# Kernel tuning notes

Hardware: AMD Instinct MI355X
Metric: run time of the kernel (lower is better)

## Reference

```python
import jax, jax.numpy as jnp
import numpy as np

H = 32        # num_attention_heads
KVH = 8       # num_key_value_heads
D = 2048      # hidden_size
HD = D // H   # head_dim = 64
GROUPS = H // KVH


def setup_inputs() -> dict:
    key = jax.random.key(0)
    k1, k2, k3, k4 = jax.random.split(key, 4)
    B, T = 2, 2048
    x = jax.random.normal(k1, (B, T, D), dtype=jnp.float32)
    wq = jax.random.normal(k2, (D, H * HD), dtype=jnp.float32) * (D ** -0.5)
    wkv = jax.random.normal(k3, (D, 2 * KVH * HD), dtype=jnp.float32) * (D ** -0.5)
    wo = jax.random.normal(k4, (H * HD, D), dtype=jnp.float32) * (D ** -0.5)
    return {"x": x, "wq": wq, "wkv": wkv, "wo": wo}


def reference(x, wq, wkv, wo):
    B, T, _ = x.shape
    scale = HD ** -0.5
    # projections
    q = (x @ wq).reshape(B, T, H, HD).transpose(0, 2, 1, 3)        # [B,H,T,hd]
    kv = x @ wkv                                                    # [B,T,2*KVH*hd]
    k, v = jnp.split(kv, 2, axis=-1)
    k = k.reshape(B, T, KVH, HD).transpose(0, 2, 1, 3)              # [B,KVH,T,hd]
    v = v.reshape(B, T, KVH, HD).transpose(0, 2, 1, 3)
    # repeat_interleave KV heads to match Q heads
    k = jnp.repeat(k, GROUPS, axis=1)                               # [B,H,T,hd]
    v = jnp.repeat(v, GROUPS, axis=1)
    scores = jnp.einsum('bhqd,bhkd->bhqk', q, k) * scale            # [B,H,T,T]
    causal = jnp.triu(jnp.ones((T, T), dtype=bool), k=1)
    scores = jnp.where(causal, -jnp.inf, scores)
    attn = jax.nn.softmax(scores, axis=-1)
    out = jnp.einsum('bhqk,bhkd->bhqd', attn, v)                    # [B,H,T,hd]
    out = out.transpose(0, 2, 1, 3).reshape(B, T, H * HD)
    return out @ wo
```

## Files before the change

### kernel.cpp

```cpp
#include <hip/hip_runtime.h>

using bf16   = __bf16;
using bf16x8 = __attribute__((ext_vector_type(8))) __bf16;
using f32x4  = __attribute__((ext_vector_type(4))) float;
using u32x4  = __attribute__((ext_vector_type(4))) unsigned;

#define T_SEQ 2048
#define NQKV 3072

__device__ __forceinline__ void async_cp16(const bf16* g, bf16* l) {
  __builtin_amdgcn_global_load_lds((__attribute__((address_space(1))) void*)(void*)g,
                                   (__attribute__((address_space(3))) void*)l, 16, 0, 0);
}

__global__ __launch_bounds__(256) void cvt_kernel(const float* __restrict__ in,
                                                  bf16* __restrict__ out) {
  long i = ((long)blockIdx.x * 256 + threadIdx.x) * 8;
  float4 a = *(const float4*)(in + i);
  float4 c = *(const float4*)(in + i + 4);
  bf16x8 v;
  v[0] = (bf16)a.x; v[1] = (bf16)a.y; v[2] = (bf16)a.z; v[3] = (bf16)a.w;
  v[4] = (bf16)c.x; v[5] = (bf16)c.y; v[6] = (bf16)c.z; v[7] = (bf16)c.w;
  *(bf16x8*)(out + i) = v;
}

__global__ __launch_bounds__(256) void transpose_cvt(const float* __restrict__ in,
                                                     bf16* __restrict__ out,
                                                     int R, int C) {
  __shared__ float tile[32][33];
  const int tc = blockIdx.x * 32;
  const int tr = blockIdx.y * 32;
  const int t = threadIdx.x;
  const int lr = t >> 5;
  const int lc = t & 31;
#pragma unroll
  for (int i = 0; i < 4; ++i)
    tile[lr + i * 8][lc] = in[(size_t)(tr + lr + i * 8) * C + tc + lc];
  __syncthreads();
#pragma unroll
  for (int i = 0; i < 4; ++i)
    out[(size_t)(tc + lr + i * 8) * R + tr + lc] = (bf16)tile[lc][lr + i * 8];
}

__global__ __launch_bounds__(256) void transpose_v(const bf16* __restrict__ in,
                                                   bf16* __restrict__ out) {
  __shared__ bf16 tile[32][33];
  const int c0 = blockIdx.x * 32;
  const int r0 = blockIdx.y * 32;
  const int t = threadIdx.x;
  const int lr = t >> 5;
  const int lc = t & 31;
#pragma unroll
  for (int i = 0; i < 4; ++i)
    tile[lr + i * 8][lc] = in[(size_t)(r0 + lr + i * 8) * NQKV + 2560 + c0 + lc];
  __syncthreads();
#pragma unroll
  for (int i = 0; i < 4; ++i) {
    int c = c0 + lr + i * 8;
    int r = r0 + lc;
    out[(size_t)((r >> 11) * 512 + c) * 2048 + (r & 2047)] = tile[lc][lr + i * 8];
  }
}

template <bool OUT_BF16>
__global__ __launch_bounds__(256, 3)
void gemm_kernel(const bf16* __restrict__ A, const bf16* __restrict__ Bt,
                 void* __restrict__ Cout, int Kdim, int Ndim) {
  __shared__ __attribute__((aligned(16))) bf16 As[128 * 64];
  __shared__ __attribute__((aligned(16))) bf16 Bs[128 * 64];
  const int tid  = threadIdx.x;
  const int lane = tid & 63;
  const int wave = tid >> 6;
  const int l16  = lane & 15;
  const int q4   = lane >> 4;
  const long m0 = (long)blockIdx.y * 128;
  const long n0 = (long)blockIdx.x * 128;
  const int wm = (wave >> 1) * 64;
  const int wn = (wave & 1) * 64;

  f32x4 acc[4][4] = {};

  for (int k0 = 0; k0 < Kdim; k0 += 64) {
    __syncthreads();
#pragma unroll
    for (int rr = 0; rr < 4; ++rr) {
      int ci  = rr * 256 + tid;
      int row = ci >> 3;
      int chp = ci & 7;
      int ch  = chp ^ (row & 7);
      async_cp16(A + (m0 + row) * (long)Kdim + k0 + ch * 8, &As[ci * 8]);
      async_cp16(Bt + (n0 + row) * (long)Kdim + k0 + ch * 8, &Bs[ci * 8]);
    }
    __syncthreads();
#pragma unroll
    for (int ks = 0; ks < 2; ++ks) {
      bf16x8 af[4], bfr[4];
#pragma unroll
      for (int mt = 0; mt < 4; ++mt) {
        int row = wm + mt * 16 + l16;
        int chp = (ks * 4 + q4) ^ (row & 7);
        af[mt] = *(const bf16x8*)&As[row * 64 + chp * 8];
      }
#pragma unroll
      for (int nt = 0; nt < 4; ++nt) {
        int row = wn + nt * 16 + l16;
        int chp = (ks * 4 + q4) ^ (row & 7);
        bfr[nt] = *(const bf16x8*)&Bs[row * 64 + chp * 8];
      }
#pragma unroll
      for (int mt = 0; mt < 4; ++mt)
#pragma unroll
        for (int nt = 0; nt < 4; ++nt)
          acc[mt][nt] = __builtin_amdgcn_mfma_f32_16x16x32_bf16(af[mt], bfr[nt],
                                                                acc[mt][nt], 0, 0, 0);
    }
  }
#pragma unroll
  for (int mt = 0; mt < 4; ++mt)
#pragma unroll
    for (int nt = 0; nt < 4; ++nt)
#pragma unroll
      for (int r = 0; r < 4; ++r) {
        long row = m0 + wm + mt * 16 + q4 * 4 + r;
        long col = n0 + wn + nt * 16 + l16;
        float v = acc[mt][nt][r];
        if constexpr (OUT_BF16)
          ((bf16*)Cout)[row * Ndim + col] = (bf16)v;
        else
          ((float*)Cout)[row * Ndim + col] = v;
      }
}

__global__ __launch_bounds__(256, 3)
void attn_kernel(const bf16* __restrict__ qkv, const bf16* __restrict__ vT,
                 bf16* __restrict__ outb) {
  __shared__ __attribute__((aligned(16))) bf16 Ks[64 * 64];
  __shared__ __attribute__((aligned(16))) bf16 Vs[64 * 64];

  const int tid  = threadIdx.x;
  const int lane = tid & 63;
  const int wave = tid >> 6;
  const int l16  = lane & 15;
  const int q4   = lane >> 4;

  const int bid = blockIdx.x;
  const int qt  = 15 - (bid >> 6);
  const int bh  = bid & 63;
  const int b   = bh >> 5;
  const int h   = bh & 31;
  const int kvh = h >> 2;
  const long rowbase = (long)b * T_SEQ;

  const int qrow0 = qt * 128;
  const int wq0   = qrow0 + wave * 32;
  const float cexp = 0.125f * 1.4426950408889634f;

  bf16x8 aq[2][2];
#pragma unroll
  for (int mt = 0; mt < 2; ++mt)
#pragma unroll
    for (int ks = 0; ks < 2; ++ks) {
      bf16x8 v = *(const bf16x8*)(qkv +
          (rowbase + wq0 + mt * 16 + l16) * (long)NQKV + h * 64 + ks * 32 + q4 * 8);
#pragma unroll
      for (int i = 0; i < 8; ++i) v[i] = (bf16)((float)v[i] * cexp);
      aq[mt][ks] = v;
    }

  bf16x8 ones_f;
#pragma unroll
  for (int i = 0; i < 8; ++i) ones_f[i] = (l16 == 0) ? (bf16)1.0f : (bf16)0.0f;

  f32x4 o[2][4] = {};
  f32x4 o_l[2] = {};

  const bf16* kbase = qkv + rowbase * (long)NQKV + 2048 + kvh * 64;
  const bf16* vbase = vT + ((long)b * 512 + kvh * 64) * 2048;

  for (int j0 = 0; j0 < qrow0 + 128; j0 += 64) {
    __syncthreads();
    {
#pragma unroll
      for (int h2 = 0; h2 < 2; ++h2) {
        int ci  = h2 * 256 + tid;
        int row = ci >> 3;
        int ch  = (ci & 7) ^ (row & 7);
        *(bf16x8*)&Ks[ci * 8] =
            *(const bf16x8*)(kbase + (long)(j0 + row) * NQKV + ch * 8);
        *(bf16x8*)&Vs[ci * 8] =
            *(const bf16x8*)(vbase + (long)row * 2048 + j0 + ch * 8);
      }
    }
    __syncthreads();
    if (j0 > wq0 + 31) continue;

    f32x4 s[2][4] = {};
#pragma unroll
    for (int ks = 0; ks < 2; ++ks) {
      bf16x8 bk[4];
#pragma unroll
      for (int nt = 0; nt < 4; ++nt) {
        int row  = nt * 16 + l16;
        int slot = (ks * 4 + q4) ^ (row & 7);
        bk[nt] = *(const bf16x8*)&Ks[row * 64 + slot * 8];
      }
#pragma unroll
      for (int mt = 0; mt < 2; ++mt)
#pragma unroll
        for (int nt = 0; nt < 4; ++nt)
          s[mt][nt] = __builtin_amdgcn_mfma_f32_16x16x32_bf16(bk[nt], aq[mt][ks],
                                                              s[mt][nt], 0, 0, 0);
    }

    if (j0 + 63 > wq0) {
#pragma unroll
      for (int mt = 0; mt < 2; ++mt)
#pragma unroll
        for (int nt = 0; nt < 4; ++nt)
#pragma unroll
          for (int r = 0; r < 4; ++r) {
            int rg = wq0 + mt * 16 + l16;
            int cg = j0 + nt * 16 + q4 * 4 + r;
            if (cg > rg) s[mt][nt][r] = -__builtin_inff();
          }
    }

    bf16x8 ap[2][2];
#pragma unroll
    for (int mt = 0; mt < 2; ++mt) {
      unsigned pk0, pk1, pk2, pk3, pk4, pk5, pk6, pk7;
      {
        float p0 = __builtin_amdgcn_exp2f(s[mt][0][0]);
        float p1 = __builtin_amdgcn_exp2f(s[mt][0][1]);
        float p2 = __builtin_amdgcn_exp2f(s[mt][0][2]);
        float p3 = __builtin_amdgcn_exp2f(s[mt][0][3]);
        asm("v_cvt_pk_bf16_f32 %0, %1, %2" : "=v"(pk0) : "v"(p0), "v"(p1));
        asm("v_cvt_pk_bf16_f32 %0, %1, %2" : "=v"(pk1) : "v"(p2), "v"(p3));
      }
      {
        float p0 = __builtin_amdgcn_exp2f(s[mt][1][0]);
        float p1 = __builtin_amdgcn_exp2f(s[mt][1][1]);
        float p2 = __builtin_amdgcn_exp2f(s[mt][1][2]);
        float p3 = __builtin_amdgcn_exp2f(s[mt][1][3]);
        asm("v_cvt_pk_bf16_f32 %0, %1, %2" : "=v"(pk2) : "v"(p0), "v"(p1));
        asm("v_cvt_pk_bf16_f32 %0, %1, %2" : "=v"(pk3) : "v"(p2), "v"(p3));
      }
      {
        float p0 = __builtin_amdgcn_exp2f(s[mt][2][0]);
        float p1 = __builtin_amdgcn_exp2f(s[mt][2][1]);
        float p2 = __builtin_amdgcn_exp2f(s[mt][2][2]);
        float p3 = __builtin_amdgcn_exp2f(s[mt][2][3]);
        asm("v_cvt_pk_bf16_f32 %0, %1, %2" : "=v"(pk4) : "v"(p0), "v"(p1));
        asm("v_cvt_pk_bf16_f32 %0, %1, %2" : "=v"(pk5) : "v"(p2), "v"(p3));
      }
      {
        float p0 = __builtin_amdgcn_exp2f(s[mt][3][0]);
        float p1 = __builtin_amdgcn_exp2f(s[mt][3][1]);
        float p2 = __builtin_amdgcn_exp2f(s[mt][3][2]);
        float p3 = __builtin_amdgcn_exp2f(s[mt][3][3]);
        asm("v_cvt_pk_bf16_f32 %0, %1, %2" : "=v"(pk6) : "v"(p0), "v"(p1));
        asm("v_cvt_pk_bf16_f32 %0, %1, %2" : "=v"(pk7) : "v"(p2), "v"(p3));
      }
      {
        unsigned a0 = pk0, b0 = pk2;
        asm("v_permlane32_swap_b32 %0, %1" : "+v"(a0), "+v"(b0));
        asm("v_permlane16_swap_b32 %0, %1" : "+v"(a0), "+v"(b0));
        unsigned a1 = pk1, b1 = pk3;
        asm("v_permlane32_swap_b32 %0, %1" : "+v"(a1), "+v"(b1));
        asm("v_permlane16_swap_b32 %0, %1" : "+v"(a1), "+v"(b1));
        u32x4 w; w.x = a0; w.y = a1; w.z = b0; w.w = b1;
        ap[mt][0] = __builtin_bit_cast(bf16x8, w);
      }
      {
        unsigned a0 = pk4, b0 = pk6;
        asm("v_permlane32_swap_b32 %0, %1" : "+v"(a0), "+v"(b0));
        asm("v_permlane16_swap_b32 %0, %1" : "+v"(a0), "+v"(b0));
        unsigned a1 = pk5, b1 = pk7;
        asm("v_permlane32_swap_b32 %0, %1" : "+v"(a1), "+v"(b1));
        asm("v_permlane16_swap_b32 %0, %1" : "+v"(a1), "+v"(b1));
        u32x4 w; w.x = a0; w.y = a1; w.z = b0; w.w = b1;
        ap[mt][1] = __builtin_bit_cast(bf16x8, w);
      }
    }

#pragma unroll
    for (int ks = 0; ks < 2; ++ks) {
      bf16x8 bv[4];
#pragma unroll
      for (int dt = 0; dt < 4; ++dt) {
        int row  = dt * 16 + l16;
        int slot = (ks * 4 + q4) ^ (row & 7);
        bv[dt] = *(const bf16x8*)&Vs[row * 64 + slot * 8];
      }
#pragma unroll
      for (int mt = 0; mt < 2; ++mt) {
#pragma unroll
        for (int dt = 0; dt < 4; ++dt)
          o[mt][dt] = __builtin_amdgcn_mfma_f32_16x16x32_bf16(ap[mt][ks], bv[dt],
                                                              o[mt][dt], 0, 0, 0);
        o_l[mt] = __builtin_amdgcn_mfma_f32_16x16x32_bf16(ap[mt][ks], ones_f,
                                                          o_l[mt], 0, 0, 0);
      }
    }
  }

#pragma unroll
  for (int mt = 0; mt < 2; ++mt) {
    float inv[4];
#pragma unroll
    for (int r = 0; r < 4; ++r) {
      float lsum = __shfl(o_l[mt][r], lane & 48);
      inv[r] = 1.0f / lsum;
    }
#pragma unroll
    for (int dt = 0; dt < 4; ++dt)
#pragma unroll
      for (int r = 0; r < 4; ++r) {
        long row = rowbase + wq0 + mt * 16 + q4 * 4 + r;
        int col = h * 64 + dt * 16 + l16;
        outb[row * 2048 + col] = (bf16)(o[mt][dt][r] * inv[r]);
      }
  }
}

extern "C" void kernel_launch(void* const* d_in, const int* in_sizes, int n_in,
                              void* d_out, int out_size, void* d_ws, size_t ws_size,
                              hipStream_t stream) {
  const float* x   = (const float*)d_in[0];
  const float* wq  = (const float*)d_in[1];
  const float* wkv = (const float*)d_in[2];
  const float* wo  = (const float*)d_in[3];
  float* out = (float*)d_out;
  char* ws = (char*)d_ws;

  bf16* xbf  = (bf16*)(ws + 0);
  bf16* w1   = (bf16*)(ws + 16777216);
  bf16* qkv  = (bf16*)(ws + 29360128);
  bf16* attn = xbf;
  bf16* vT   = w1;

  const size_t need_parallel = 54525952u + 8388608u;
  bf16* woT;
  bool woT_early;
  if (ws_size >= need_parallel) {
    woT = (bf16*)(ws + 54525952);
    woT_early = true;
  } else {
    woT = qkv;
    woT_early = false;
  }

  cvt_kernel<<<4096, 256, 0, stream>>>(x, xbf);
  transpose_cvt<<<dim3(64, 64), 256, 0, stream>>>(wq, w1, 2048, 2048);
  transpose_cvt<<<dim3(32, 64), 256, 0, stream>>>(wkv, w1 + 2048L * 2048, 2048, 1024);
  if (woT_early)
    transpose_cvt<<<dim3(64, 64), 256, 0, stream>>>(wo, woT, 2048, 2048);

  gemm_kernel<true><<<dim3(24, 32), 256, 0, stream>>>(xbf, w1, (void*)qkv, 2048, 3072);

  transpose_v<<<dim3(16, 128), 256, 0, stream>>>(qkv, vT);

  attn_kernel<<<1024, 256, 0, stream>>>(qkv, vT, attn);

  if (!woT_early)
    transpose_cvt<<<dim3(64, 64), 256, 0, stream>>>(wo, woT, 2048, 2048);

  gemm_kernel<false><<<dim3(16, 32), 256, 0, stream>>>(attn, woT, (void*)out, 2048, 2048);
}
```

Baseline: 258.9 us.

## Replace GEMM with 8-wave double-buffered larger-tile kernel with async prefetch

Replaces the 128x128 single-buffered GEMM with a 512-thread kernel using 256xBN tiles and double-buffered LDS. The next K tile loads asynchronously while MFMAs run on the current one, synchronised with explicit vmcnt waits and raw barriers, and MFMA phases get raised wave priority. This targets the exposed global-load latency and the redundant operand traffic of the smaller tiles, at the cost of more LDS and registers per block. It also means fewer blocks per GEMM (192 and 256), which could leave CUs underused.

```diff
diff --git a/kernel.cpp b/kernel.cpp
--- a/kernel.cpp
+++ b/kernel.cpp
@@ -62,63 +62,142 @@
   }
 }
 
-template <bool OUT_BF16>
-__global__ __launch_bounds__(256, 3)
-void gemm_kernel(const bf16* __restrict__ A, const bf16* __restrict__ Bt,
-                 void* __restrict__ Cout, int Kdim, int Ndim) {
-  __shared__ __attribute__((aligned(16))) bf16 As[128 * 64];
-  __shared__ __attribute__((aligned(16))) bf16 Bs[128 * 64];
+template <int KDIM, int BN, bool OUT_BF16>
+__global__ __launch_bounds__(512, 2)
+void gemm8_kernel(const bf16* __restrict__ A, const bf16* __restrict__ Bt,
+                  void* __restrict__ Cout, int Ndim) {
+  constexpr int NTILES = KDIM / 64;
+  constexpr int NFR = BN / 64;
+  __shared__ __attribute__((aligned(16))) bf16 As[2][256 * 64];
+  __shared__ __attribute__((aligned(16))) bf16 Bs[2][BN * 64];
+
   const int tid  = threadIdx.x;
   const int lane = tid & 63;
   const int wave = tid >> 6;
   const int l16  = lane & 15;
   const int q4   = lane >> 4;
-  const long m0 = (long)blockIdx.y * 128;
-  const long n0 = (long)blockIdx.x * 128;
-  const int wm = (wave >> 1) * 64;
-  const int wn = (wave & 1) * 64;
-
-  f32x4 acc[4][4] = {};
-
-  for (int k0 = 0; k0 < Kdim; k0 += 64) {
-    __syncthreads();
+  const int wm   = (wave >> 2) * 128;
+  const int wn   = (wave & 3) * (BN / 4);
+
+  const long m0 = (long)blockIdx.y * 256;
+  const long n0 = (long)blockIdx.x * BN;
+  const bf16* Ag = A + m0 * (long)KDIM;
+  const bf16* Bg = Bt + n0 * (long)KDIM;
+
+  f32x4 acc[8][NFR] = {};
+
+  auto stage = [&](int buf, int kt) {
+    const long k0 = (long)kt * 64;
 #pragma unroll
     for (int rr = 0; rr < 4; ++rr) {
-      int ci  = rr * 256 + tid;
+      int ci = rr * 512 + tid;
       int row = ci >> 3;
-      int chp = ci & 7;
-      int ch  = chp ^ (row & 7);
-      async_cp16(A + (m0 + row) * (long)Kdim + k0 + ch * 8, &As[ci * 8]);
-      async_cp16(Bt + (n0 + row) * (long)Kdim + k0 + ch * 8, &Bs[ci * 8]);
-    }
-    __syncthreads();
-#pragma unroll
-    for (int ks = 0; ks < 2; ++ks) {
-      bf16x8 af[4], bfr[4];
-#pragma unroll
-      for (int mt = 0; mt < 4; ++mt) {
-        int row = wm + mt * 16 + l16;
-        int chp = (ks * 4 + q4) ^ (row & 7);
-        af[mt] = *(const bf16x8*)&As[row * 64 + chp * 8];
-      }
-#pragma unroll
-      for (int nt = 0; nt < 4; ++nt) {
-        int row = wn + nt * 16 + l16;
-        int chp = (ks * 4 + q4) ^ (row & 7);
-        bfr[nt] = *(const bf16x8*)&Bs[row * 64 + chp * 8];
-      }
-#pragma unroll
-      for (int mt = 0; mt < 4; ++mt)
-#pragma unroll
-        for (int nt = 0; nt < 4; ++nt)
-          acc[mt][nt] = __builtin_amdgcn_mfma_f32_16x16x32_bf16(af[mt], bfr[nt],
-                                                                acc[mt][nt], 0, 0, 0);
-    }
+      int ch = (ci & 7) ^ (row & 7);
+      async_cp16(Ag + (long)row * KDIM + k0 + ch * 8, &As[buf][ci * 8]);
+    }
+#pragma unroll
+    for (int rr = 0; rr < BN / 64; ++rr) {
+      int ci = rr * 512 + tid;
+      int row = ci >> 3;
+      int ch = (ci & 7) ^ (row & 7);
+      async_cp16(Bg + (long)row * KDIM + k0 + ch * 8, &Bs[buf][ci * 8]);
+    }
+  };
+
+  stage(0, 0);
+  stage(1, 1);
+
+  for (int t = 0; t < NTILES; ++t) {
+    const int cur = t & 1;
+    if (t < NTILES - 1) {
+      if constexpr (BN == 256) asm volatile("s_waitcnt vmcnt(8)" ::: "memory");
+      else                     asm volatile("s_waitcnt vmcnt(6)" ::: "memory");
+    } else {
+      asm volatile("s_waitcnt vmcnt(0)" ::: "memory");
+    }
+    __builtin_amdgcn_s_barrier();
+
+    bf16x8 a0[4], b0[NFR];
+#pragma unroll
+    for (int mt = 0; mt < 4; ++mt) {
+      int row = wm + mt * 16 + l16;
+      int slot = q4 ^ (row & 7);
+      a0[mt] = *(const bf16x8*)&As[cur][row * 64 + slot * 8];
+    }
+#pragma unroll
+    for (int nt = 0; nt < NFR; ++nt) {
+      int row = wn + nt * 16 + l16;
+      int slot = q4 ^ (row & 7);
+      b0[nt] = *(const bf16x8*)&Bs[cur][row * 64 + slot * 8];
+    }
+    __builtin_amdgcn_s_setprio(1);
+#pragma unroll
+    for (int mt = 0; mt < 4; ++mt)
+#pragma unroll
+      for (int nt = 0; nt < NFR; ++nt)
+        acc[mt][nt] = __builtin_amdgcn_mfma_f32_16x16x32_bf16(a0[mt], b0[nt],
+                                                              acc[mt][nt], 0, 0, 0);
+    __builtin_amdgcn_s_setprio(0);
+    bf16x8 a0h[4];
+#pragma unroll
+    for (int mt = 0; mt < 4; ++mt) {
+      int row = wm + 64 + mt * 16 + l16;
+      int slot = q4 ^ (row & 7);
+      a0h[mt] = *(const bf16x8*)&As[cur][row * 64 + slot * 8];
+    }
+    __builtin_amdgcn_s_setprio(1);
+#pragma unroll
+    for (int mt = 0; mt < 4; ++mt)
+#pragma unroll
+      for (int nt = 0; nt < NFR; ++nt)
+        acc[4 + mt][nt] = __builtin_amdgcn_mfma_f32_16x16x32_bf16(a0h[mt], b0[nt],
+                                                                  acc[4 + mt][nt], 0, 0, 0);
+    __builtin_amdgcn_s_setprio(0);
+
+    bf16x8 a1[4], a1h[4], b1[NFR];
+#pragma unroll
+    for (int mt = 0; mt < 4; ++mt) {
+      int row = wm + mt * 16 + l16;
+      int slot = (4 + q4) ^ (row & 7);
+      a1[mt] = *(const bf16x8*)&As[cur][row * 64 + slot * 8];
+    }
+#pragma unroll
+    for (int mt = 0; mt < 4; ++mt) {
+      int row = wm + 64 + mt * 16 + l16;
+      int slot = (4 + q4) ^ (row & 7);
+      a1h[mt] = *(const bf16x8*)&As[cur][row * 64 + slot * 8];
+    }
+#pragma unroll
+    for (int nt = 0; nt < NFR; ++nt) {
+      int row = wn + nt * 16 + l16;
+      int slot = (4 + q4) ^ (row & 7);
+      b1[nt] = *(const bf16x8*)&Bs[cur][row * 64 + slot * 8];
+    }
+    asm volatile("s_waitcnt lgkmcnt(0)" ::: "memory");
+    __builtin_amdgcn_sched_barrier(0);
+    __builtin_amdgcn_s_barrier();
+    if (t + 2 < NTILES) stage(cur, t + 2);
+
+    __builtin_amdgcn_s_setprio(1);
+#pragma unroll
+    for (int mt = 0; mt < 4; ++mt)
+#pragma unroll
+      for (int nt = 0; nt < NFR; ++nt)
+        acc[mt][nt] = __builtin_amdgcn_mfma_f32_16x16x32_bf16(a1[mt], b1[nt],
+                                                              acc[mt][nt], 0, 0, 0);
+#pragma unroll
+    for (int mt = 0; mt < 4; ++mt)
+#pragma unroll
+      for (int nt = 0; nt < NFR; ++nt)
+        acc[4 + mt][nt] = __builtin_amdgcn_mfma_f32_16x16x32_bf16(a1h[mt], b1[nt],
+                                                                  acc[4 + mt][nt], 0, 0, 0);
+    __builtin_amdgcn_s_setprio(0);
   }
-#pragma unroll
-  for (int mt = 0; mt < 4; ++mt)
-#pragma unroll
-    for (int nt = 0; nt < 4; ++nt)
+
+#pragma unroll
+  for (int mt = 0; mt < 8; ++mt)
+#pragma unroll
+    for (int nt = 0; nt < NFR; ++nt)
 #pragma unroll
       for (int r = 0; r < 4; ++r) {
         long row = m0 + wm + mt * 16 + q4 * 4 + r;
@@ -356,7 +435,7 @@
   if (woT_early)
     transpose_cvt<<<dim3(64, 64), 256, 0, stream>>>(wo, woT, 2048, 2048);
 
-  gemm_kernel<true><<<dim3(24, 32), 256, 0, stream>>>(xbf, w1, (void*)qkv, 2048, 3072);
+  gemm8_kernel<2048, 256, true><<<dim3(12, 16), 512, 0, stream>>>(xbf, w1, (void*)qkv, 3072);
 
   transpose_v<<<dim3(16, 128), 256, 0, stream>>>(qkv, vT);
 
@@ -365,5 +444,5 @@
   if (!woT_early)
     transpose_cvt<<<dim3(64, 64), 256, 0, stream>>>(wo, woT, 2048, 2048);
 
-  gemm_kernel<false><<<dim3(16, 32), 256, 0, stream>>>(attn, woT, (void*)out, 2048, 2048);
-}
+  gemm8_kernel<2048, 128, false><<<dim3(16, 16), 512, 0, stream>>>(attn, woT, (void*)out, 2048);
+}
```

Measured after the change: 260.6 us. No clear change (+0.7%).

## Merge preprocessing launches and register-prefetch next K/V tile in attention

Applied to the files above, without the earlier changes.

The x conversion and the three weight transposes now run as one launch, using a z-dimension to select the job, instead of four separate launches. This removes launch gaps and lets the small kernels fill the GPU together. In the attention loop, the next K/V tile is loaded into registers while the current tile is computed, then written to LDS at the start of the next iteration, so global load latency overlaps with MFMA work. The cost is extra registers, which could lower occupancy, and idle blocks in the z=2 slice of the merged grid.

```diff
diff --git a/kernel.cpp b/kernel.cpp
--- a/kernel.cpp
+++ b/kernel.cpp
@@ -13,15 +13,40 @@
                                    (__attribute__((address_space(3))) void*)l, 16, 0, 0);
 }
 
-__global__ __launch_bounds__(256) void cvt_kernel(const float* __restrict__ in,
-                                                  bf16* __restrict__ out) {
-  long i = ((long)blockIdx.x * 256 + threadIdx.x) * 8;
-  float4 a = *(const float4*)(in + i);
-  float4 c = *(const float4*)(in + i + 4);
-  bf16x8 v;
-  v[0] = (bf16)a.x; v[1] = (bf16)a.y; v[2] = (bf16)a.z; v[3] = (bf16)a.w;
-  v[4] = (bf16)c.x; v[5] = (bf16)c.y; v[6] = (bf16)c.z; v[7] = (bf16)c.w;
-  *(bf16x8*)(out + i) = v;
+__global__ __launch_bounds__(256) void prep_kernel(
+    const float* __restrict__ x, bf16* __restrict__ xbf,
+    const float* __restrict__ wq, const float* __restrict__ wkv,
+    const float* __restrict__ wo, bf16* __restrict__ w1,
+    bf16* __restrict__ woT) {
+  const int z = blockIdx.z;
+  if (z == 0) {
+    long i = (((long)blockIdx.y * 64 + blockIdx.x) * 256 + threadIdx.x) * 8;
+    float4 a = *(const float4*)(x + i);
+    float4 c = *(const float4*)(x + i + 4);
+    bf16x8 v;
+    v[0] = (bf16)a.x; v[1] = (bf16)a.y; v[2] = (bf16)a.z; v[3] = (bf16)a.w;
+    v[4] = (bf16)c.x; v[5] = (bf16)c.y; v[6] = (bf16)c.z; v[7] = (bf16)c.w;
+    *(bf16x8*)(xbf + i) = v;
+    return;
+  }
+  const float* in; bf16* out; int R, C;
+  if (z == 1)      { in = wq;  out = w1;                R = 2048; C = 2048; }
+  else if (z == 2) { if (blockIdx.x >= 32) return;
+                     in = wkv; out = w1 + 2048L * 2048; R = 2048; C = 1024; }
+  else             { in = wo;  out = woT;               R = 2048; C = 2048; }
+  __shared__ float tile[32][33];
+  const int tc = blockIdx.x * 32;
+  const int tr = blockIdx.y * 32;
+  const int t = threadIdx.x;
+  const int lr = t >> 5;
+  const int lc = t & 31;
+#pragma unroll
+  for (int i = 0; i < 4; ++i)
+    tile[lr + i * 8][lc] = in[(size_t)(tr + lr + i * 8) * C + tc + lc];
+  __syncthreads();
+#pragma unroll
+  for (int i = 0; i < 4; ++i)
+    out[(size_t)(tc + lr + i * 8) * R + tr + lc] = (bf16)tile[lc][lr + i * 8];
 }
 
 __global__ __launch_bounds__(256) void transpose_cvt(const float* __restrict__ in,
@@ -177,21 +202,35 @@
   const bf16* kbase = qkv + rowbase * (long)NQKV + 2048 + kvh * 64;
   const bf16* vbase = vT + ((long)b * 512 + kvh * 64) * 2048;
 
-  for (int j0 = 0; j0 < qrow0 + 128; j0 += 64) {
+  const int ntiles = (qrow0 + 128) >> 6;
+
+  bf16x8 kr[2], vr[2];
+#pragma unroll
+  for (int h2 = 0; h2 < 2; ++h2) {
+    int ci = h2 * 256 + tid, row = ci >> 3, ch = (ci & 7) ^ (row & 7);
+    kr[h2] = *(const bf16x8*)(kbase + (long)row * NQKV + ch * 8);
+    vr[h2] = *(const bf16x8*)(vbase + (long)row * 2048 + ch * 8);
+  }
+
+  for (int t = 0; t < ntiles; ++t) {
+    const int j0 = t * 64;
     __syncthreads();
-    {
+#pragma unroll
+    for (int h2 = 0; h2 < 2; ++h2) {
+      int ci = h2 * 256 + tid;
+      *(bf16x8*)&Ks[ci * 8] = kr[h2];
+      *(bf16x8*)&Vs[ci * 8] = vr[h2];
+    }
+    __syncthreads();
+    if (t + 1 < ntiles) {
+      const int jn = j0 + 64;
 #pragma unroll
       for (int h2 = 0; h2 < 2; ++h2) {
-        int ci  = h2 * 256 + tid;
-        int row = ci >> 3;
-        int ch  = (ci & 7) ^ (row & 7);
-        *(bf16x8*)&Ks[ci * 8] =
-            *(const bf16x8*)(kbase + (long)(j0 + row) * NQKV + ch * 8);
-        *(bf16x8*)&Vs[ci * 8] =
-            *(const bf16x8*)(vbase + (long)row * 2048 + j0 + ch * 8);
-      }
-    }
-    __syncthreads();
+        int ci = h2 * 256 + tid, row = ci >> 3, ch = (ci & 7) ^ (row & 7);
+        kr[h2] = *(const bf16x8*)(kbase + (long)(jn + row) * NQKV + ch * 8);
+        vr[h2] = *(const bf16x8*)(vbase + (long)row * 2048 + jn + ch * 8);
+      }
+    }
     if (j0 > wq0 + 31) continue;
 
     f32x4 s[2][4] = {};
@@ -350,11 +389,8 @@
     woT_early = false;
   }
 
-  cvt_kernel<<<4096, 256, 0, stream>>>(x, xbf);
-  transpose_cvt<<<dim3(64, 64), 256, 0, stream>>>(wq, w1, 2048, 2048);
-  transpose_cvt<<<dim3(32, 64), 256, 0, stream>>>(wkv, w1 + 2048L * 2048, 2048, 1024);
-  if (woT_early)
-    transpose_cvt<<<dim3(64, 64), 256, 0, stream>>>(wo, woT, 2048, 2048);
+  prep_kernel<<<dim3(64, 64, woT_early ? 4 : 3), 256, 0, stream>>>(
+      x, xbf, wq, wkv, wo, w1, woT);
 
   gemm_kernel<true><<<dim3(24, 32), 256, 0, stream>>>(xbf, w1, (void*)qkv, 2048, 3072);
 
```

Result: no change. 258.7 us (-0.0%).
